# Kernel tuning notes

Hardware: AMD Instinct MI355X
Metric: run time of the kernel (lower is better)

Reference implementation:

```python
import jax, jax.numpy as jnp
import numpy as np

B, S, D = 1, 2048, 1024   # batch, seq_len, d_model
E, F, TOP_K = 8, 4096, 2  # num_experts, d_ff, top_k


def setup_inputs() -> dict:
    key = jax.random.key(0)
    k0, k1, k2, k3, k4 = jax.random.split(key, 5)
    s = 0.02
    x = jax.random.normal(k0, (B, S, D), jnp.float32)
    Wr = jax.random.normal(k1, (D, E), jnp.float32) * s          # router
    W1 = jax.random.normal(k2, (E, D, F), jnp.float32) * s       # gate proj per expert
    W3 = jax.random.normal(k3, (E, D, F), jnp.float32) * s       # up proj per expert
    W2 = jax.random.normal(k4, (E, F, D), jnp.float32) * s       # down proj per expert
    return {"x": x, "Wr": Wr, "W1": W1, "W2": W2, "W3": W3}


def reference(x, Wr, W1, W2, W3):
    b, s, d = x.shape
    e = Wr.shape[1]
    xt = x.reshape(b * s, d)                       # [T, D]
    logits = xt @ Wr                               # [T, E]
    top_v, top_i = jax.lax.top_k(logits, TOP_K)    # [T, K]
    probs = jax.nn.softmax(top_v, axis=-1)         # softmax over selected experts
    # combine[t, e] = prob of expert e for token t (0 if not selected)
    combine = jnp.sum(probs[..., None] * jax.nn.one_hot(top_i, e, dtype=xt.dtype), axis=1)  # [T, E]
    # SwiGLU FFN per expert (dense grouped-GEMM form of the gather/scatter loop)
    h = jnp.einsum('td,edf->etf', xt, W1)          # [E, T, F]
    g = jnp.einsum('td,edf->etf', xt, W3)          # [E, T, F]
    y = jnp.einsum('etf,efd->etd', jax.nn.silu(h) * g, W2)  # [E, T, D]
    out = jnp.einsum('etd,te->td', y, combine)     # weighted combine
    return out.reshape(b, s, d)
```

## Files before the change

### kernel.cpp

```cpp
#include <hip/hip_runtime.h>
#include <hip/hip_bf16.h>

#define T_TOK 2048
#define DDIM  1024
#define NEXP  8
#define FDIM  4096

typedef __attribute__((ext_vector_type(8))) short bf16x8;
typedef __attribute__((ext_vector_type(4))) float f32x4;

#define SBW(n) ((((n) >> 3) ^ (n)) & 7)

__device__ __forceinline__ unsigned short f2b(float f) {
  union { float f; unsigned u; } v; v.f = f;
  unsigned r = v.u + 0x7FFF + ((v.u >> 16) & 1);
  return (unsigned short)(r >> 16);
}
__device__ __forceinline__ float b2f(unsigned short s) {
  union { unsigned u; float f; } v; v.u = ((unsigned)s) << 16;
  return v.f;
}
__device__ __forceinline__ unsigned cvtpk(float lo, float hi) {
  unsigned r;
  asm("v_cvt_pk_bf16_f32 %0, %1, %2" : "=v"(r) : "v"(lo), "v"(hi));
  return r;
}
__device__ __forceinline__ void gl16(const unsigned short* g, unsigned short* l) {
  __builtin_amdgcn_global_load_lds(
      (const __attribute__((address_space(1))) unsigned int*)(const void*)g,
      (__attribute__((address_space(3))) unsigned int*)(void*)l, 16, 0, 0);
}
__device__ __forceinline__ bf16x8 pack8(const float4* br, int c) {
  union { bf16x8 v; unsigned u[4]; } p;
  p.u[0] = cvtpk((&br[0].x)[c], (&br[1].x)[c]);
  p.u[1] = cvtpk((&br[2].x)[c], (&br[3].x)[c]);
  p.u[2] = cvtpk((&br[4].x)[c], (&br[5].x)[c]);
  p.u[3] = cvtpk((&br[6].x)[c], (&br[7].x)[c]);
  return p.v;
}

__global__ void router_kernel(const float* __restrict__ x, const float* __restrict__ Wr,
                              int* __restrict__ cnt, int* __restrict__ tok,
                              float* __restrict__ prb) {
  int t = (blockIdx.x * blockDim.x + threadIdx.x) >> 6;
  int lane = threadIdx.x & 63;
  if (t >= T_TOK) return;
  const float* xr = x + (size_t)t * DDIM;
  float acc[NEXP];
#pragma unroll
  for (int e = 0; e < NEXP; ++e) acc[e] = 0.f;
#pragma unroll
  for (int i = 0; i < 4; ++i) {
    int d0 = lane * 16 + i * 4;
    float4 xv = *reinterpret_cast<const float4*>(xr + d0);
#pragma unroll
    for (int j = 0; j < 4; ++j) {
      float xd = (&xv.x)[j];
      float4 w0 = *reinterpret_cast<const float4*>(Wr + (size_t)(d0 + j) * NEXP);
      float4 w1 = *reinterpret_cast<const float4*>(Wr + (size_t)(d0 + j) * NEXP + 4);
      acc[0] += xd * w0.x; acc[1] += xd * w0.y; acc[2] += xd * w0.z; acc[3] += xd * w0.w;
      acc[4] += xd * w1.x; acc[5] += xd * w1.y; acc[6] += xd * w1.z; acc[7] += xd * w1.w;
    }
  }
#pragma unroll
  for (int off = 32; off >= 1; off >>= 1)
#pragma unroll
    for (int e = 0; e < NEXP; ++e) acc[e] += __shfl_down(acc[e], off);
  if (lane == 0) {
    float v0 = -1e30f, v1 = -1e30f; int i0 = 0, i1 = 0;
#pragma unroll
    for (int e = 0; e < NEXP; ++e) {
      float v = acc[e];
      if (v > v0)      { v1 = v0; i1 = i0; v0 = v; i0 = e; }
      else if (v > v1) { v1 = v; i1 = e; }
    }
    float e1 = __expf(v1 - v0);
    float p0 = 1.f / (1.f + e1);
    float p1 = e1 * p0;
    int s0 = atomicAdd(&cnt[i0], 1);
    tok[i0 * T_TOK + s0] = t; prb[i0 * T_TOK + s0] = p0;
    int s1 = atomicAdd(&cnt[i1], 1);
    tok[i1 * T_TOK + s1] = t; prb[i1 * T_TOK + s1] = p1;
  }
}

__global__ void cvt_x_kernel(const float* __restrict__ in, unsigned short* __restrict__ o) {
  size_t i = ((size_t)blockIdx.x * 256 + threadIdx.x) * 8;
  float4 a = *reinterpret_cast<const float4*>(in + i);
  float4 b = *reinterpret_cast<const float4*>(in + i + 4);
  bf16x8 p;
  p[0] = (short)f2b(a.x); p[1] = (short)f2b(a.y); p[2] = (short)f2b(a.z); p[3] = (short)f2b(a.w);
  p[4] = (short)f2b(b.x); p[5] = (short)f2b(b.y); p[6] = (short)f2b(b.z); p[7] = (short)f2b(b.w);
  *reinterpret_cast<bf16x8*>(o + i) = p;
}

__global__ __launch_bounds__(256, 2)
void gemm1ab_kernel(const unsigned short* __restrict__ xb,
                    const float* __restrict__ W1, const float* __restrict__ W3,
                    const int* __restrict__ cnt, const int* __restrict__ tok,
                    unsigned short* __restrict__ act) {
  const int e = blockIdx.z;
  const int cn = cnt[e];
  const int r0 = blockIdx.y * 128;
  if (r0 >= cn) return;
  const int n0 = blockIdx.x * 64;
  int off = 0;
#pragma unroll
  for (int i = 0; i < NEXP; ++i) off += (i < e) ? cnt[i] : 0;

  __shared__ __align__(16) unsigned short sA[2][128 * 64];
  __shared__ __align__(16) unsigned short sB1[2][64 * 64];
  __shared__ __align__(16) unsigned short sB3[2][64 * 64];

  const int tid = threadIdx.x;
  const int lane = tid & 63;
  const int wid = tid >> 6;
  const int wm = wid >> 1, wn = wid & 1;

  const unsigned short* asrc[4];
#pragma unroll
  for (int i = 0; i < 4; ++i) {
    int row = (4 * wid + i) * 8 + (lane >> 3);
    int slot = r0 + row; if (slot >= cn) slot = cn - 1;
    int tk = tok[e * T_TOK + slot];
    int sl = (lane & 7) ^ (row & 7);
    asrc[i] = xb + (size_t)tk * DDIM + sl * 8;
  }

  const int lt = tid & 127;
  const int ko = lt >> 4;
  const int nc = (lt & 15) * 4;
  const float* bp = ((tid < 128) ? W1 : W3) + ((size_t)e * DDIM + 8 * ko) * FDIM + n0 + nc;
  unsigned short* wb = (tid < 128) ? &sB1[0][0] : &sB3[0][0];
  int woff[4];
#pragma unroll
  for (int c = 0; c < 4; ++c) woff[c] = (nc + c) * 64 + ((ko ^ SBW(nc + c)) * 8);

  float4 br[8];
#define LOADB1(K0)                                                              \
  _Pragma("unroll") for (int r = 0; r < 8; ++r)                                 \
      br[r] = *reinterpret_cast<const float4*>(bp + (size_t)((K0) + r) * FDIM);
#define WRITEB1(BUF)                                                            \
  _Pragma("unroll") for (int c = 0; c < 4; ++c)                                 \
      *reinterpret_cast<bf16x8*>(wb + (BUF) * 4096 + woff[c]) = pack8(br, c);
#define STAGEA1(K0, BUF)                                                        \
  _Pragma("unroll") for (int i = 0; i < 4; ++i)                                 \
      gl16(asrc[i] + (K0), &sA[BUF][(4 * wid + i) * 512]);

  f32x4 ah[4][2], ag[4][2];
#pragma unroll
  for (int m = 0; m < 4; ++m)
#pragma unroll
    for (int n = 0; n < 2; ++n) { ah[m][n] = (f32x4){0,0,0,0}; ag[m][n] = (f32x4){0,0,0,0}; }

  LOADB1(0);
  STAGEA1(0, 0);
  WRITEB1(0);
  LOADB1(64);
  __syncthreads();

  int cur = 0;
  for (int k0 = 0; k0 < DDIM; k0 += 64, cur ^= 1) {
    const int nxt = cur ^ 1;
    if (k0 + 64 < DDIM) {
      STAGEA1(k0 + 64, nxt);
      WRITEB1(nxt);
      if (k0 + 128 < DDIM) LOADB1(k0 + 128);
    }
#pragma unroll
    for (int kk = 0; kk < 2; ++kk) {
      int kc8 = kk * 4 + (lane >> 4);
      bf16x8 a[4], b1[2], b3[2];
#pragma unroll
      for (int m = 0; m < 4; ++m) {
        int row = wm * 64 + m * 16 + (lane & 15);
        a[m] = *reinterpret_cast<const bf16x8*>(&sA[cur][row * 64 + ((kc8 ^ (row & 7)) * 8)]);
      }
#pragma unroll
      for (int n = 0; n < 2; ++n) {
        int rowb = wn * 32 + n * 16 + (lane & 15);
        int offb = rowb * 64 + ((kc8 ^ SBW(rowb)) * 8);
        b1[n] = *reinterpret_cast<const bf16x8*>(&sB1[cur][offb]);
        b3[n] = *reinterpret_cast<const bf16x8*>(&sB3[cur][offb]);
      }
#pragma unroll
      for (int m = 0; m < 4; ++m)
#pragma unroll
        for (int n = 0; n < 2; ++n) {
          ah[m][n] = __builtin_amdgcn_mfma_f32_16x16x32_bf16(a[m], b1[n], ah[m][n], 0, 0, 0);
          ag[m][n] = __builtin_amdgcn_mfma_f32_16x16x32_bf16(a[m], b3[n], ag[m][n], 0, 0, 0);
        }
    }
    __syncthreads();
  }
#pragma unroll
  for (int m = 0; m < 4; ++m)
#pragma unroll
    for (int j = 0; j < 4; ++j) {
      int rloc = wm * 64 + m * 16 + (lane >> 4) * 4 + j;
      int s = r0 + rloc;
      if (s < cn) {
        unsigned short* orow = act + (size_t)(off + s) * FDIM + n0 + wn * 32 + (lane & 15);
#pragma unroll
        for (int n = 0; n < 2; ++n) {
          float hv = ah[m][n][j];
          float gv = ag[m][n][j];
          float sg = hv / (1.f + __expf(-hv));
          orow[n * 16] = f2b(sg * gv);
        }
      }
    }
}

__global__ __launch_bounds__(256, 2)
void gemm2d_kernel(const unsigned short* __restrict__ act, const float* __restrict__ W2,
                   const int* __restrict__ cnt, const int* __restrict__ tok,
                   const float* __restrict__ prb, float* __restrict__ out) {
  const int e = blockIdx.z >> 2;
  const int sp = blockIdx.z & 3;
  const int cn = cnt[e];
  const int r0 = blockIdx.y * 128;
  if (r0 >= cn) return;
  const int n0 = blockIdx.x * 128;
  const int kbase = sp * (FDIM / 4);
  int off = 0;
#pragma unroll
  for (int i = 0; i < NEXP; ++i) off += (i < e) ? cnt[i] : 0;

  __shared__ __align__(16) unsigned short sA[2][128 * 64];
  __shared__ __align__(16) unsigned short sB[2][128 * 64];

  const int tid = threadIdx.x;
  const int lane = tid & 63;
  const int wid = tid >> 6;
  const int wm = wid >> 1, wn = wid & 1;

  const unsigned short* asrc[4];
#pragma unroll
  for (int i = 0; i < 4; ++i) {
    int row = (4 * wid + i) * 8 + (lane >> 3);
    int sl = (lane & 7) ^ (row & 7);
    asrc[i] = act + (size_t)(off + r0 + row) * FDIM + kbase + sl * 8;
  }

  const int ko = tid >> 5;
  const int nc = (tid & 31) * 4;
  const float* bp = W2 + ((size_t)e * FDIM + kbase + 8 * ko) * DDIM + n0 + nc;
  int woff[4];
#pragma unroll
  for (int c = 0; c < 4; ++c) woff[c] = (nc + c) * 64 + ((ko ^ SBW(nc + c)) * 8);

  float4 br[8];
#define LOADB2(K0)                                                              \
  _Pragma("unroll") for (int r = 0; r < 8; ++r)                                 \
      br[r] = *reinterpret_cast<const float4*>(bp + (size_t)((K0) + r) * DDIM);
#define WRITEB2(BUF)                                                            \
  _Pragma("unroll") for (int c = 0; c < 4; ++c)                                 \
      *reinterpret_cast<bf16x8*>(&sB[BUF][woff[c]]) = pack8(br, c);
#define STAGEA2(K0, BUF)                                                        \
  _Pragma("unroll") for (int i = 0; i < 4; ++i)                                 \
      gl16(asrc[i] + (K0), &sA[BUF][(4 * wid + i) * 512]);

  f32x4 acc[4][4];
#pragma unroll
  for (int m = 0; m < 4; ++m)
#pragma unroll
    for (int n = 0; n < 4; ++n) acc[m][n] = (f32x4){0,0,0,0};

  LOADB2(0);
  STAGEA2(0, 0);
  WRITEB2(0);
  LOADB2(64);
  __syncthreads();

  int cur = 0;
  for (int k0 = 0; k0 < FDIM / 4; k0 += 64, cur ^= 1) {
    const int nxt = cur ^ 1;
    if (k0 + 64 < FDIM / 4) {
      STAGEA2(k0 + 64, nxt);
      WRITEB2(nxt);
      if (k0 + 128 < FDIM / 4) LOADB2(k0 + 128);
    }
#pragma unroll
    for (int kk = 0; kk < 2; ++kk) {
      int kc8 = kk * 4 + (lane >> 4);
      bf16x8 a[4], b[4];
#pragma unroll
      for (int m = 0; m < 4; ++m) {
        int row = wm * 64 + m * 16 + (lane & 15);
        a[m] = *reinterpret_cast<const bf16x8*>(&sA[cur][row * 64 + ((kc8 ^ (row & 7)) * 8)]);
      }
#pragma unroll
      for (int n = 0; n < 4; ++n) {
        int rowb = wn * 64 + n * 16 + (lane & 15);
        b[n] = *reinterpret_cast<const bf16x8*>(&sB[cur][rowb * 64 + ((kc8 ^ SBW(rowb)) * 8)]);
      }
#pragma unroll
      for (int m = 0; m < 4; ++m)
#pragma unroll
        for (int n = 0; n < 4; ++n)
          acc[m][n] = __builtin_amdgcn_mfma_f32_16x16x32_bf16(a[m], b[n], acc[m][n], 0, 0, 0);
    }
    __syncthreads();
  }
#pragma unroll
  for (int m = 0; m < 4; ++m)
#pragma unroll
    for (int j = 0; j < 4; ++j) {
      int rloc = wm * 64 + m * 16 + (lane >> 4) * 4 + j;
      int s = r0 + rloc;
      if (s < cn) {
        int tkn = tok[e * T_TOK + s];
        float p = prb[e * T_TOK + s];
        float* orow = out + (size_t)tkn * DDIM + n0 + wn * 64 + (lane & 15);
#pragma unroll
        for (int n = 0; n < 4; ++n) atomicAdd(&orow[n * 16], p * acc[m][n][j]);
      }
    }
}

extern "C" void kernel_launch(void* const* d_in, const int* in_sizes, int n_in,
                              void* d_out, int out_size, void* d_ws, size_t ws_size,
                              hipStream_t stream) {
  const float* x  = (const float*)d_in[0];
  const float* Wr = (const float*)d_in[1];
  const float* W1 = (const float*)d_in[2];
  const float* W2 = (const float*)d_in[3];
  const float* W3 = (const float*)d_in[4];
  float* out = (float*)d_out;

  char* ws = (char*)d_ws;
  int*   cnt = (int*)ws;
  int*   tok = (int*)(ws + 1024);
  float* prb = (float*)(ws + 1024 + 65536);
  unsigned short* xb  = (unsigned short*)(ws + 256 * 1024);
  unsigned short* act = xb + (size_t)T_TOK * DDIM;

  hipMemsetAsync(cnt, 0, NEXP * sizeof(int), stream);
  hipMemsetAsync(d_out, 0, (size_t)out_size * sizeof(float), stream);

  router_kernel<<<T_TOK / 4, 256, 0, stream>>>(x, Wr, cnt, tok, prb);
  cvt_x_kernel<<<(T_TOK * DDIM) / (256 * 8), 256, 0, stream>>>(x, xb);
  gemm1ab_kernel<<<dim3(FDIM / 64, 16, NEXP), 256, 0, stream>>>(xb, W1, W3, cnt, tok, act);
  gemm2d_kernel<<<dim3(DDIM / 128, 16, NEXP * 4), 256, 0, stream>>>(act, W2, cnt, tok, prb, out);
}
```

Before: 322.4 us.

## Unify expert GEMMs into one 256x256-tile template kernel with split gate/up passes

Replaces the fused gate+up GEMM and the down GEMM with a single templated 512-thread kernel using 256x256 output tiles, chosen by epilogue mode. The gate/up projection now runs as two passes: the first writes the up projection to a bf16 intermediate buffer, the second computes the gate projection and applies SiLU times the stored value. The larger tiles are meant to improve operand reuse and cut redundant conversion of the fp32 weights. In exchange there is an extra global round trip for the intermediate, the gathered token rows are loaded twice, and per-expert row tiles carry more padding waste. The B-tile register prefetch is also shortened from two stages ahead to one.

```diff
diff --git a/kernel.cpp b/kernel.cpp
--- a/kernel.cpp
+++ b/kernel.cpp
@@ -5,6 +5,7 @@
 #define DDIM  1024
 #define NEXP  8
 #define FDIM  4096
+#define ROWS  (4096 + 256)
 
 typedef __attribute__((ext_vector_type(8))) short bf16x8;
 typedef __attribute__((ext_vector_type(4))) float f32x4;
@@ -94,227 +95,137 @@
   *reinterpret_cast<bf16x8*>(o + i) = p;
 }
 
-__global__ __launch_bounds__(256, 2)
-void gemm1ab_kernel(const unsigned short* __restrict__ xb,
-                    const float* __restrict__ W1, const float* __restrict__ W3,
-                    const int* __restrict__ cnt, const int* __restrict__ tok,
-                    unsigned short* __restrict__ act) {
-  const int e = blockIdx.z;
+template <int EPI>
+__global__ __launch_bounds__(512, 2)
+void gemm_big(const unsigned short* __restrict__ Abase, const float* __restrict__ W,
+              const int* __restrict__ cnt, const int* __restrict__ tok,
+              const float* __restrict__ prb, unsigned short* __restrict__ gbuf,
+              unsigned short* __restrict__ obuf_bf, float* __restrict__ obuf_f32,
+              int ldb , int wrows ) {
+  const int e  = (EPI == 2) ? (blockIdx.z >> 2) : blockIdx.z;
+  const int sp = (EPI == 2) ? (blockIdx.z & 3) : 0;
   const int cn = cnt[e];
-  const int r0 = blockIdx.y * 128;
+  const int r0 = blockIdx.y * 256;
   if (r0 >= cn) return;
-  const int n0 = blockIdx.x * 64;
+  const int n0 = blockIdx.x * 256;
+  const int kbase = sp * 1024;
   int off = 0;
 #pragma unroll
   for (int i = 0; i < NEXP; ++i) off += (i < e) ? cnt[i] : 0;
 
-  __shared__ __align__(16) unsigned short sA[2][128 * 64];
-  __shared__ __align__(16) unsigned short sB1[2][64 * 64];
-  __shared__ __align__(16) unsigned short sB3[2][64 * 64];
+  __shared__ __align__(16) unsigned short sA[2][256 * 64];
+  __shared__ __align__(16) unsigned short sB[2][256 * 64];
 
   const int tid = threadIdx.x;
   const int lane = tid & 63;
   const int wid = tid >> 6;
-  const int wm = wid >> 1, wn = wid & 1;
+  const int wm = wid >> 2;
+  const int wn = wid & 3;
 
   const unsigned short* asrc[4];
 #pragma unroll
   for (int i = 0; i < 4; ++i) {
-    int row = (4 * wid + i) * 8 + (lane >> 3);
-    int slot = r0 + row; if (slot >= cn) slot = cn - 1;
-    int tk = tok[e * T_TOK + slot];
+    int row = wid * 32 + i * 8 + (lane >> 3);
     int sl = (lane & 7) ^ (row & 7);
-    asrc[i] = xb + (size_t)tk * DDIM + sl * 8;
-  }
-
-  const int lt = tid & 127;
-  const int ko = lt >> 4;
-  const int nc = (lt & 15) * 4;
-  const float* bp = ((tid < 128) ? W1 : W3) + ((size_t)e * DDIM + 8 * ko) * FDIM + n0 + nc;
-  unsigned short* wb = (tid < 128) ? &sB1[0][0] : &sB3[0][0];
+    if (EPI == 2) {
+      asrc[i] = Abase + (size_t)(off + r0 + row) * FDIM + kbase + sl * 8;
+    } else {
+      int slot = r0 + row; if (slot >= cn) slot = cn - 1;
+      int tk = tok[e * T_TOK + slot];
+      asrc[i] = Abase + (size_t)tk * DDIM + sl * 8;
+    }
+  }
+
+  const int ko = wid;
+  const int nc = lane * 4;
+  const float* bp = W + ((size_t)e * wrows + kbase + 8 * ko) * ldb + n0 + nc;
   int woff[4];
 #pragma unroll
   for (int c = 0; c < 4; ++c) woff[c] = (nc + c) * 64 + ((ko ^ SBW(nc + c)) * 8);
 
   float4 br[8];
-#define LOADB1(K0)                                                              \
+#define LOADB(K0)                                                               \
   _Pragma("unroll") for (int r = 0; r < 8; ++r)                                 \
-      br[r] = *reinterpret_cast<const float4*>(bp + (size_t)((K0) + r) * FDIM);
-#define WRITEB1(BUF)                                                            \
+      br[r] = *reinterpret_cast<const float4*>(bp + (size_t)((K0) + r) * ldb);
+#define WRITEB(BUF)                                                             \
   _Pragma("unroll") for (int c = 0; c < 4; ++c)                                 \
-      *reinterpret_cast<bf16x8*>(wb + (BUF) * 4096 + woff[c]) = pack8(br, c);
-#define STAGEA1(K0, BUF)                                                        \
+      *reinterpret_cast<bf16x8*>(&sB[BUF][woff[c]]) = pack8(br, c);
+#define STAGEA(K0, BUF)                                                         \
   _Pragma("unroll") for (int i = 0; i < 4; ++i)                                 \
-      gl16(asrc[i] + (K0), &sA[BUF][(4 * wid + i) * 512]);
-
-  f32x4 ah[4][2], ag[4][2];
-#pragma unroll
-  for (int m = 0; m < 4; ++m)
-#pragma unroll
-    for (int n = 0; n < 2; ++n) { ah[m][n] = (f32x4){0,0,0,0}; ag[m][n] = (f32x4){0,0,0,0}; }
-
-  LOADB1(0);
-  STAGEA1(0, 0);
-  WRITEB1(0);
-  LOADB1(64);
+      gl16(asrc[i] + (K0), &sA[BUF][(wid * 4 + i) * 512]);
+
+  f32x4 acc[8][4];
+#pragma unroll
+  for (int m = 0; m < 8; ++m)
+#pragma unroll
+    for (int n = 0; n < 4; ++n) acc[m][n] = (f32x4){0.f, 0.f, 0.f, 0.f};
+
+  LOADB(0);
+  STAGEA(0, 0);
+  WRITEB(0);
   __syncthreads();
 
   int cur = 0;
-  for (int k0 = 0; k0 < DDIM; k0 += 64, cur ^= 1) {
+  for (int k0 = 0; k0 < 1024; k0 += 64, cur ^= 1) {
     const int nxt = cur ^ 1;
-    if (k0 + 64 < DDIM) {
-      STAGEA1(k0 + 64, nxt);
-      WRITEB1(nxt);
-      if (k0 + 128 < DDIM) LOADB1(k0 + 128);
+    const bool more = (k0 + 64 < 1024);
+    if (more) {
+      LOADB(k0 + 64);
+      STAGEA(k0 + 64, nxt);
     }
 #pragma unroll
     for (int kk = 0; kk < 2; ++kk) {
       int kc8 = kk * 4 + (lane >> 4);
-      bf16x8 a[4], b1[2], b3[2];
-#pragma unroll
-      for (int m = 0; m < 4; ++m) {
-        int row = wm * 64 + m * 16 + (lane & 15);
+      bf16x8 a[8], b[4];
+#pragma unroll
+      for (int m = 0; m < 8; ++m) {
+        int row = wm * 128 + m * 16 + (lane & 15);
         a[m] = *reinterpret_cast<const bf16x8*>(&sA[cur][row * 64 + ((kc8 ^ (row & 7)) * 8)]);
       }
 #pragma unroll
-      for (int n = 0; n < 2; ++n) {
-        int rowb = wn * 32 + n * 16 + (lane & 15);
-        int offb = rowb * 64 + ((kc8 ^ SBW(rowb)) * 8);
-        b1[n] = *reinterpret_cast<const bf16x8*>(&sB1[cur][offb]);
-        b3[n] = *reinterpret_cast<const bf16x8*>(&sB3[cur][offb]);
+      for (int n = 0; n < 4; ++n) {
+        int col = wn * 64 + n * 16 + (lane & 15);
+        b[n] = *reinterpret_cast<const bf16x8*>(&sB[cur][col * 64 + ((kc8 ^ SBW(col)) * 8)]);
       }
 #pragma unroll
-      for (int m = 0; m < 4; ++m)
-#pragma unroll
-        for (int n = 0; n < 2; ++n) {
-          ah[m][n] = __builtin_amdgcn_mfma_f32_16x16x32_bf16(a[m], b1[n], ah[m][n], 0, 0, 0);
-          ag[m][n] = __builtin_amdgcn_mfma_f32_16x16x32_bf16(a[m], b3[n], ag[m][n], 0, 0, 0);
-        }
-    }
+      for (int m = 0; m < 8; ++m)
+#pragma unroll
+        for (int n = 0; n < 4; ++n)
+          acc[m][n] = __builtin_amdgcn_mfma_f32_16x16x32_bf16(a[m], b[n], acc[m][n], 0, 0, 0);
+    }
+    if (more) WRITEB(nxt);
     __syncthreads();
   }
-#pragma unroll
-  for (int m = 0; m < 4; ++m)
+
+#pragma unroll
+  for (int m = 0; m < 8; ++m)
 #pragma unroll
     for (int j = 0; j < 4; ++j) {
-      int rloc = wm * 64 + m * 16 + (lane >> 4) * 4 + j;
+      int rloc = wm * 128 + m * 16 + (lane >> 4) * 4 + j;
       int s = r0 + rloc;
       if (s < cn) {
-        unsigned short* orow = act + (size_t)(off + s) * FDIM + n0 + wn * 32 + (lane & 15);
-#pragma unroll
-        for (int n = 0; n < 2; ++n) {
-          float hv = ah[m][n][j];
-          float gv = ag[m][n][j];
-          float sg = hv / (1.f + __expf(-hv));
-          orow[n * 16] = f2b(sg * gv);
+        int colb = n0 + wn * 64 + (lane & 15);
+        if (EPI == 0) {
+          unsigned short* orow = gbuf + (size_t)(off + s) * FDIM + colb;
+#pragma unroll
+          for (int n = 0; n < 4; ++n) orow[n * 16] = f2b(acc[m][n][j]);
+        } else if (EPI == 1) {
+          const unsigned short* grow = gbuf + (size_t)(off + s) * FDIM + colb;
+          unsigned short* orow = obuf_bf + (size_t)(off + s) * FDIM + colb;
+#pragma unroll
+          for (int n = 0; n < 4; ++n) {
+            float hv = acc[m][n][j];
+            float gv = b2f(grow[n * 16]);
+            float sg = hv / (1.f + __expf(-hv));
+            orow[n * 16] = f2b(sg * gv);
+          }
+        } else {
+          int tkn = tok[e * T_TOK + s];
+          float p = prb[e * T_TOK + s];
+          float* orow = obuf_f32 + (size_t)tkn * DDIM + colb;
+#pragma unroll
+          for (int n = 0; n < 4; ++n) atomicAdd(&orow[n * 16], p * acc[m][n][j]);
         }
-      }
-    }
-}
-
-__global__ __launch_bounds__(256, 2)
-void gemm2d_kernel(const unsigned short* __restrict__ act, const float* __restrict__ W2,
-                   const int* __restrict__ cnt, const int* __restrict__ tok,
-                   const float* __restrict__ prb, float* __restrict__ out) {
-  const int e = blockIdx.z >> 2;
-  const int sp = blockIdx.z & 3;
-  const int cn = cnt[e];
-  const int r0 = blockIdx.y * 128;
-  if (r0 >= cn) return;
-  const int n0 = blockIdx.x * 128;
-  const int kbase = sp * (FDIM / 4);
-  int off = 0;
-#pragma unroll
-  for (int i = 0; i < NEXP; ++i) off += (i < e) ? cnt[i] : 0;
-
-  __shared__ __align__(16) unsigned short sA[2][128 * 64];
-  __shared__ __align__(16) unsigned short sB[2][128 * 64];
-
-  const int tid = threadIdx.x;
-  const int lane = tid & 63;
-  const int wid = tid >> 6;
-  const int wm = wid >> 1, wn = wid & 1;
-
-  const unsigned short* asrc[4];
-#pragma unroll
-  for (int i = 0; i < 4; ++i) {
-    int row = (4 * wid + i) * 8 + (lane >> 3);
-    int sl = (lane & 7) ^ (row & 7);
-    asrc[i] = act + (size_t)(off + r0 + row) * FDIM + kbase + sl * 8;
-  }
-
-  const int ko = tid >> 5;
-  const int nc = (tid & 31) * 4;
-  const float* bp = W2 + ((size_t)e * FDIM + kbase + 8 * ko) * DDIM + n0 + nc;
-  int woff[4];
-#pragma unroll
-  for (int c = 0; c < 4; ++c) woff[c] = (nc + c) * 64 + ((ko ^ SBW(nc + c)) * 8);
-
-  float4 br[8];
-#define LOADB2(K0)                                                              \
-  _Pragma("unroll") for (int r = 0; r < 8; ++r)                                 \
-      br[r] = *reinterpret_cast<const float4*>(bp + (size_t)((K0) + r) * DDIM);
-#define WRITEB2(BUF)                                                            \
-  _Pragma("unroll") for (int c = 0; c < 4; ++c)                                 \
-      *reinterpret_cast<bf16x8*>(&sB[BUF][woff[c]]) = pack8(br, c);
-#define STAGEA2(K0, BUF)                                                        \
-  _Pragma("unroll") for (int i = 0; i < 4; ++i)                                 \
-      gl16(asrc[i] + (K0), &sA[BUF][(4 * wid + i) * 512]);
-
-  f32x4 acc[4][4];
-#pragma unroll
-  for (int m = 0; m < 4; ++m)
-#pragma unroll
-    for (int n = 0; n < 4; ++n) acc[m][n] = (f32x4){0,0,0,0};
-
-  LOADB2(0);
-  STAGEA2(0, 0);
-  WRITEB2(0);
-  LOADB2(64);
-  __syncthreads();
-
-  int cur = 0;
-  for (int k0 = 0; k0 < FDIM / 4; k0 += 64, cur ^= 1) {
-    const int nxt = cur ^ 1;
-    if (k0 + 64 < FDIM / 4) {
-      STAGEA2(k0 + 64, nxt);
-      WRITEB2(nxt);
-      if (k0 + 128 < FDIM / 4) LOADB2(k0 + 128);
-    }
-#pragma unroll
-    for (int kk = 0; kk < 2; ++kk) {
-      int kc8 = kk * 4 + (lane >> 4);
-      bf16x8 a[4], b[4];
-#pragma unroll
-      for (int m = 0; m < 4; ++m) {
-        int row = wm * 64 + m * 16 + (lane & 15);
-        a[m] = *reinterpret_cast<const bf16x8*>(&sA[cur][row * 64 + ((kc8 ^ (row & 7)) * 8)]);
-      }
-#pragma unroll
-      for (int n = 0; n < 4; ++n) {
-        int rowb = wn * 64 + n * 16 + (lane & 15);
-        b[n] = *reinterpret_cast<const bf16x8*>(&sB[cur][rowb * 64 + ((kc8 ^ SBW(rowb)) * 8)]);
-      }
-#pragma unroll
-      for (int m = 0; m < 4; ++m)
-#pragma unroll
-        for (int n = 0; n < 4; ++n)
-          acc[m][n] = __builtin_amdgcn_mfma_f32_16x16x32_bf16(a[m], b[n], acc[m][n], 0, 0, 0);
-    }
-    __syncthreads();
-  }
-#pragma unroll
-  for (int m = 0; m < 4; ++m)
-#pragma unroll
-    for (int j = 0; j < 4; ++j) {
-      int rloc = wm * 64 + m * 16 + (lane >> 4) * 4 + j;
-      int s = r0 + rloc;
-      if (s < cn) {
-        int tkn = tok[e * T_TOK + s];
-        float p = prb[e * T_TOK + s];
-        float* orow = out + (size_t)tkn * DDIM + n0 + wn * 64 + (lane & 15);
-#pragma unroll
-        for (int n = 0; n < 4; ++n) atomicAdd(&orow[n * 16], p * acc[m][n][j]);
       }
     }
 }
@@ -334,13 +245,19 @@
   int*   tok = (int*)(ws + 1024);
   float* prb = (float*)(ws + 1024 + 65536);
   unsigned short* xb  = (unsigned short*)(ws + 256 * 1024);
-  unsigned short* act = xb + (size_t)T_TOK * DDIM;
+  unsigned short* g   = xb + (size_t)T_TOK * DDIM;
+  unsigned short* act = g + (size_t)ROWS * FDIM;
 
   hipMemsetAsync(cnt, 0, NEXP * sizeof(int), stream);
   hipMemsetAsync(d_out, 0, (size_t)out_size * sizeof(float), stream);
 
   router_kernel<<<T_TOK / 4, 256, 0, stream>>>(x, Wr, cnt, tok, prb);
   cvt_x_kernel<<<(T_TOK * DDIM) / (256 * 8), 256, 0, stream>>>(x, xb);
-  gemm1ab_kernel<<<dim3(FDIM / 64, 16, NEXP), 256, 0, stream>>>(xb, W1, W3, cnt, tok, act);
-  gemm2d_kernel<<<dim3(DDIM / 128, 16, NEXP * 4), 256, 0, stream>>>(act, W2, cnt, tok, prb, out);
-}
+
+  gemm_big<0><<<dim3(FDIM / 256, 8, NEXP), 512, 0, stream>>>(
+      xb, W3, cnt, tok, nullptr, g, nullptr, nullptr, FDIM, DDIM);
+  gemm_big<1><<<dim3(FDIM / 256, 8, NEXP), 512, 0, stream>>>(
+      xb, W1, cnt, tok, nullptr, g, act, nullptr, FDIM, DDIM);
+  gemm_big<2><<<dim3(DDIM / 256, 8, NEXP * 4), 512, 0, stream>>>(
+      act, W2, cnt, tok, prb, nullptr, nullptr, out, DDIM, FDIM);
+}
```

Measured after the change: 531.1 us. +64.7%, slower.

## Single-buffer B tiles with manual waitcnt barriers and raise occupancy to three blocks

Applied to the files above, without the earlier changes.

Both expert GEMM kernels now keep a single LDS buffer for the converted fp32 weight tile while keeping A double-buffered via direct global-to-LDS loads. The loop is restructured: write B, issue the next B and A loads, then a hand-written barrier that waits only for the older vector memory ops (vmcnt 12) and all LDS ops. Compute runs under raised wave priority, and a plain barrier closes each iteration. The smaller LDS footprint allows launch bounds of three blocks per CU, aiming for more latency hiding. The risks are register pressure from the tighter occupancy bound and correctness that hinges on the hard-coded vmcnt count. The last iteration also issues a wrapped-around load that is never used.

```diff
diff --git a/kernel.cpp b/kernel.cpp
--- a/kernel.cpp
+++ b/kernel.cpp
@@ -5,6 +5,7 @@
 #define DDIM  1024
 #define NEXP  8
 #define FDIM  4096
+#define ROWS  (4096 + 256)
 
 typedef __attribute__((ext_vector_type(8))) short bf16x8;
 typedef __attribute__((ext_vector_type(4))) float f32x4;
@@ -38,6 +39,15 @@
   p.u[3] = cvtpk((&br[6].x)[c], (&br[7].x)[c]);
   return p.v;
 }
+#define BAR_VM12_LGKM0()                                          \
+  __builtin_amdgcn_sched_barrier(0);                              \
+  asm volatile("s_waitcnt vmcnt(12) lgkmcnt(0)" ::: "memory");    \
+  __builtin_amdgcn_s_barrier();                                   \
+  __builtin_amdgcn_sched_barrier(0)
+#define BAR_PLAIN()                                               \
+  __builtin_amdgcn_sched_barrier(0);                              \
+  __builtin_amdgcn_s_barrier();                                   \
+  __builtin_amdgcn_sched_barrier(0)
 
 __global__ void router_kernel(const float* __restrict__ x, const float* __restrict__ Wr,
                               int* __restrict__ cnt, int* __restrict__ tok,
@@ -94,7 +104,7 @@
   *reinterpret_cast<bf16x8*>(o + i) = p;
 }
 
-__global__ __launch_bounds__(256, 2)
+__global__ __launch_bounds__(256, 3)
 void gemm1ab_kernel(const unsigned short* __restrict__ xb,
                     const float* __restrict__ W1, const float* __restrict__ W3,
                     const int* __restrict__ cnt, const int* __restrict__ tok,
@@ -109,8 +119,8 @@
   for (int i = 0; i < NEXP; ++i) off += (i < e) ? cnt[i] : 0;
 
   __shared__ __align__(16) unsigned short sA[2][128 * 64];
-  __shared__ __align__(16) unsigned short sB1[2][64 * 64];
-  __shared__ __align__(16) unsigned short sB3[2][64 * 64];
+  __shared__ __align__(16) unsigned short sB1[64 * 64];
+  __shared__ __align__(16) unsigned short sB3[64 * 64];
 
   const int tid = threadIdx.x;
   const int lane = tid & 63;
@@ -131,7 +141,7 @@
   const int ko = lt >> 4;
   const int nc = (lt & 15) * 4;
   const float* bp = ((tid < 128) ? W1 : W3) + ((size_t)e * DDIM + 8 * ko) * FDIM + n0 + nc;
-  unsigned short* wb = (tid < 128) ? &sB1[0][0] : &sB3[0][0];
+  unsigned short* wb = (tid < 128) ? sB1 : sB3;
   int woff[4];
 #pragma unroll
   for (int c = 0; c < 4; ++c) woff[c] = (nc + c) * 64 + ((ko ^ SBW(nc + c)) * 8);
@@ -140,9 +150,9 @@
 #define LOADB1(K0)                                                              \
   _Pragma("unroll") for (int r = 0; r < 8; ++r)                                 \
       br[r] = *reinterpret_cast<const float4*>(bp + (size_t)((K0) + r) * FDIM);
-#define WRITEB1(BUF)                                                            \
+#define WRITEB1()                                                               \
   _Pragma("unroll") for (int c = 0; c < 4; ++c)                                 \
-      *reinterpret_cast<bf16x8*>(wb + (BUF) * 4096 + woff[c]) = pack8(br, c);
+      *reinterpret_cast<bf16x8*>(wb + woff[c]) = pack8(br, c);
 #define STAGEA1(K0, BUF)                                                        \
   _Pragma("unroll") for (int i = 0; i < 4; ++i)                                 \
       gl16(asrc[i] + (K0), &sA[BUF][(4 * wid + i) * 512]);
@@ -155,18 +165,15 @@
 
   LOADB1(0);
   STAGEA1(0, 0);
-  WRITEB1(0);
-  LOADB1(64);
-  __syncthreads();
 
   int cur = 0;
   for (int k0 = 0; k0 < DDIM; k0 += 64, cur ^= 1) {
-    const int nxt = cur ^ 1;
-    if (k0 + 64 < DDIM) {
-      STAGEA1(k0 + 64, nxt);
-      WRITEB1(nxt);
-      if (k0 + 128 < DDIM) LOADB1(k0 + 128);
-    }
+    WRITEB1();
+    const int kn = (k0 + 64) & (DDIM - 1);
+    LOADB1(kn);
+    STAGEA1(kn, cur ^ 1);
+    BAR_VM12_LGKM0();
+    __builtin_amdgcn_s_setprio(1);
 #pragma unroll
     for (int kk = 0; kk < 2; ++kk) {
       int kc8 = kk * 4 + (lane >> 4);
@@ -180,8 +187,8 @@
       for (int n = 0; n < 2; ++n) {
         int rowb = wn * 32 + n * 16 + (lane & 15);
         int offb = rowb * 64 + ((kc8 ^ SBW(rowb)) * 8);
-        b1[n] = *reinterpret_cast<const bf16x8*>(&sB1[cur][offb]);
-        b3[n] = *reinterpret_cast<const bf16x8*>(&sB3[cur][offb]);
+        b1[n] = *reinterpret_cast<const bf16x8*>(&sB1[offb]);
+        b3[n] = *reinterpret_cast<const bf16x8*>(&sB3[offb]);
       }
 #pragma unroll
       for (int m = 0; m < 4; ++m)
@@ -191,7 +198,8 @@
           ag[m][n] = __builtin_amdgcn_mfma_f32_16x16x32_bf16(a[m], b3[n], ag[m][n], 0, 0, 0);
         }
     }
-    __syncthreads();
+    __builtin_amdgcn_s_setprio(0);
+    BAR_PLAIN();
   }
 #pragma unroll
   for (int m = 0; m < 4; ++m)
@@ -212,7 +220,7 @@
     }
 }
 
-__global__ __launch_bounds__(256, 2)
+__global__ __launch_bounds__(256, 3)
 void gemm2d_kernel(const unsigned short* __restrict__ act, const float* __restrict__ W2,
                    const int* __restrict__ cnt, const int* __restrict__ tok,
                    const float* __restrict__ prb, float* __restrict__ out) {
@@ -228,7 +236,7 @@
   for (int i = 0; i < NEXP; ++i) off += (i < e) ? cnt[i] : 0;
 
   __shared__ __align__(16) unsigned short sA[2][128 * 64];
-  __shared__ __align__(16) unsigned short sB[2][128 * 64];
+  __shared__ __align__(16) unsigned short sB[128 * 64];
 
   const int tid = threadIdx.x;
   const int lane = tid & 63;
@@ -254,9 +262,9 @@
 #define LOADB2(K0)                                                              \
   _Pragma("unroll") for (int r = 0; r < 8; ++r)                                 \
       br[r] = *reinterpret_cast<const float4*>(bp + (size_t)((K0) + r) * DDIM);
-#define WRITEB2(BUF)                                                            \
+#define WRITEB2()                                                               \
   _Pragma("unroll") for (int c = 0; c < 4; ++c)                                 \
-      *reinterpret_cast<bf16x8*>(&sB[BUF][woff[c]]) = pack8(br, c);
+      *reinterpret_cast<bf16x8*>(&sB[woff[c]]) = pack8(br, c);
 #define STAGEA2(K0, BUF)                                                        \
   _Pragma("unroll") for (int i = 0; i < 4; ++i)                                 \
       gl16(asrc[i] + (K0), &sA[BUF][(4 * wid + i) * 512]);
@@ -269,18 +277,15 @@
 
   LOADB2(0);
   STAGEA2(0, 0);
-  WRITEB2(0);
-  LOADB2(64);
-  __syncthreads();
 
   int cur = 0;
   for (int k0 = 0; k0 < FDIM / 4; k0 += 64, cur ^= 1) {
-    const int nxt = cur ^ 1;
-    if (k0 + 64 < FDIM / 4) {
-      STAGEA2(k0 + 64, nxt);
-      WRITEB2(nxt);
-      if (k0 + 128 < FDIM / 4) LOADB2(k0 + 128);
-    }
+    WRITEB2();
+    const int kn = (k0 + 64) & (FDIM / 4 - 1);
+    LOADB2(kn);
+    STAGEA2(kn, cur ^ 1);
+    BAR_VM12_LGKM0();
+    __builtin_amdgcn_s_setprio(1);
 #pragma unroll
     for (int kk = 0; kk < 2; ++kk) {
       int kc8 = kk * 4 + (lane >> 4);
@@ -292,8 +297,8 @@
       }
 #pragma unroll
       for (int n = 0; n < 4; ++n) {
-        int rowb = wn * 64 + n * 16 + (lane & 15);
-        b[n] = *reinterpret_cast<const bf16x8*>(&sB[cur][rowb * 64 + ((kc8 ^ SBW(rowb)) * 8)]);
+        int col = wn * 64 + n * 16 + (lane & 15);
+        b[n] = *reinterpret_cast<const bf16x8*>(&sB[col * 64 + ((kc8 ^ SBW(col)) * 8)]);
       }
 #pragma unroll
       for (int m = 0; m < 4; ++m)
@@ -301,7 +306,8 @@
         for (int n = 0; n < 4; ++n)
           acc[m][n] = __builtin_amdgcn_mfma_f32_16x16x32_bf16(a[m], b[n], acc[m][n], 0, 0, 0);
     }
-    __syncthreads();
+    __builtin_amdgcn_s_setprio(0);
+    BAR_PLAIN();
   }
 #pragma unroll
   for (int m = 0; m < 4; ++m)
```

New measurement: 316.9 us. Within noise of the previous version (-1.7%).
